# Performance work log

Measured on AMD Instinct MI355X. Metric: run time of the kernel, lower is better.

The kernel has to match this reference:

```python
import jax, jax.numpy as jnp
import numpy as np

N = 100000      # nodes
E = 3200000     # edges
F_IN = 128      # input feature dim
H = 256         # hidden dim
K = 30          # num_cluster
REG = 0.01      # regularizer coefficient


def _uniform(key, shape, fan_in):
    s = 1.0 / np.sqrt(fan_in)
    return jax.random.uniform(key, shape, jnp.float32, -s, s)


def setup_inputs() -> dict:
    key = jax.random.key(0)
    ks = jax.random.split(key, 11)
    x = jax.random.normal(ks[0], (N, F_IN), jnp.float32)
    edge_index = jax.random.randint(ks[1], (2, E), 0, N, jnp.int32)
    edge_attr = jax.random.uniform(ks[2], (E,), jnp.float32)
    return dict(
        x=x, edge_index=edge_index, edge_attr=edge_attr,
        W_conv1=_uniform(ks[3], (F_IN, H), F_IN), b_conv1=jnp.zeros((H,), jnp.float32),
        W_lin1=_uniform(ks[4], (F_IN, H), F_IN),  b_lin1=_uniform(ks[5], (H,), F_IN),
        W_conv2=_uniform(ks[6], (H, K), H),       b_conv2=jnp.zeros((K,), jnp.float32),
        W_lin2=_uniform(ks[7], (H, K), H),        b_lin2=_uniform(ks[8], (K,), H),
    )


def gcn_conv(x, W, b, row, col, w):
    """PyG GCNConv: symmetric-normalized, edge-weighted aggregation with self-loops (weight 1)."""
    n = x.shape[0]
    deg = jax.ops.segment_sum(w, col, num_segments=n) + 1.0  # self-loop weight 1
    dis = jax.lax.rsqrt(deg)                                  # deg > 0 always (self-loop)
    norm = dis[row] * w * dis[col]                            # [E]
    h = x @ W                                                 # [n, out]
    agg = jax.ops.segment_sum(norm[:, None] * h[row], col, num_segments=n)
    agg = agg + (dis * dis)[:, None] * h                      # self-loop contribution
    return agg + b


def reference(x, edge_index, edge_attr,
              W_conv1, b_conv1, W_lin1, b_lin1,
              W_conv2, b_conv2, W_lin2, b_lin2):
    row, col = edge_index[0], edge_index[1]
    # dropout is identity in eval mode
    h = jax.nn.relu(gcn_conv(x, W_conv1, b_conv1, row, col, edge_attr) + x @ W_lin1 + b_lin1)
    out = gcn_conv(h, W_conv2, b_conv2, row, col, edge_attr) + h @ W_lin2 + b_lin2
    FX = jnp.clip(jax.nn.softmax(out, axis=-1), 1e-9, 1.0 - 1e-9)  # [N, K]

    # modularity loss
    m = jnp.sum(edge_attr)
    degree = jax.ops.segment_sum(edge_attr, row, num_segments=x.shape[0])  # [N]
    connectivity = jnp.sum(edge_attr * jnp.sum(FX[row, :-1] * FX[col, :-1], axis=-1))
    s = jnp.sum(FX * degree[:, None], axis=0)[:-1]
    avg_connectivity = jnp.dot(s, s) / (2.0 * m)
    modularity = -(connectivity - avg_connectivity) / (2.0 * m)

    # collapse regularizer
    reg = (jnp.sqrt(jnp.sum(jnp.sum(FX, axis=0) ** 2) + 1e-9)
           * (FX.shape[-1] ** 0.5) / FX.shape[0] - 1.0)
    return FX, modularity + REG * reg
```

## Files before the change

kernel.cpp:

```cpp
#include <hip/hip_runtime.h>
#include <hip/hip_bf16.h>
#include <math.h>

#define N_NODES 100000
#define N_EDGES 3200000
#define F_IN 128
#define HID 256
#define KCL 30
#define NCOPY 8

typedef unsigned int uint;
typedef unsigned short ushort;
typedef unsigned char uchar;
typedef __attribute__((ext_vector_type(8))) short bf16x8;
typedef __attribute__((ext_vector_type(4))) float f32x4;
typedef __attribute__((ext_vector_type(2))) float f32x2;

static __device__ __forceinline__ float bf2f(ushort u) {
  return __uint_as_float(((uint)u) << 16);
}
static __device__ __forceinline__ float bf2f_hi(uint u) {
  return __uint_as_float(u & 0xFFFF0000u);
}
static __device__ __forceinline__ ushort f2bf(float f) {
  uint u = __float_as_uint(f);
  uint r = (u + 0x7FFF + ((u >> 16) & 1)) >> 16;
  return (ushort)r;
}

static __device__ __forceinline__ uchar f2fp8(float f) {
#if __has_builtin(__builtin_amdgcn_cvt_pk_fp8_f32)
  return (uchar)(__builtin_amdgcn_cvt_pk_fp8_f32(f, f, 0, false) & 0xFF);
#else
  uint u = __float_as_uint(f);
  uint s = (u >> 24) & 0x80u;
  float a = fabsf(f);
  if (a >= 448.f) return (uchar)(s | 0x7E);
  if (a < 0.015625f) {
    int q = (int)rintf(a * 512.f);
    return (uchar)(s | (q > 8 ? 8 : q));
  }
  int e = ((int)((u >> 23) & 0xFF)) - 127;
  float step = __uint_as_float((uint)(127 + e - 3) << 23);
  int q = (int)rintf(a / step);
  if (q == 16) { e += 1; q = 8; }
  return (uchar)(s | ((e + 7) << 3) | (q - 8));
#endif
}
static __device__ __forceinline__ float fp82f_sw(uchar b) {
  uint s = ((uint)(b & 0x80u)) << 24;
  uint em = b & 0x7Fu;
  float mag;
  if ((em >> 3) == 0) mag = (float)em * 0.001953125f;
  else mag = __uint_as_float((((em >> 3) + 120) << 23) | ((em & 7u) << 20));
  return __uint_as_float(s | __float_as_uint(mag));
}
static __device__ __forceinline__ void fp8x4_dec(uint u, float* o) {
#if __has_builtin(__builtin_amdgcn_cvt_pk_f32_fp8)
  f32x2 lo = __builtin_amdgcn_cvt_pk_f32_fp8((int)u, false);
  f32x2 hi = __builtin_amdgcn_cvt_pk_f32_fp8((int)u, true);
  o[0] = lo.x; o[1] = lo.y; o[2] = hi.x; o[3] = hi.y;
#else
  o[0] = fp82f_sw(u & 0xFF); o[1] = fp82f_sw((u >> 8) & 0xFF);
  o[2] = fp82f_sw((u >> 16) & 0xFF); o[3] = fp82f_sw((u >> 24) & 0xFF);
#endif
}


__global__ __launch_bounds__(256) void k_cnt8(const int* __restrict__ ei,
                                              int* __restrict__ cnt8) {
  int e = blockIdx.x * 256 + threadIdx.x;
  int g = blockIdx.x & (NCOPY - 1);
  int c = ei[N_EDGES + e];
  atomicAdd(cnt8 + (size_t)g * N_NODES + c, 1);
}

__global__ __launch_bounds__(1024) void k_scanA(const int* __restrict__ cnt8,
                                                int* __restrict__ off8,
                                                int* __restrict__ blocktot) {
  __shared__ int wsum[16];
  const int t = threadIdx.x;
  const int lane = t & 63, wid = t >> 6;
  int node = blockIdx.x * 1024 + t;
  int v[NCOPY];
  int tot = 0;
  if (node < N_NODES) {
    #pragma unroll
    for (int g = 0; g < NCOPY; ++g) {
      int x = cnt8[(size_t)g * N_NODES + node];
      v[g] = tot;
      tot += x;
    }
  } else {
    #pragma unroll
    for (int g = 0; g < NCOPY; ++g) v[g] = 0;
  }
  int x = tot;
  #pragma unroll
  for (int o = 1; o < 64; o <<= 1) {
    int y = __shfl_up(x, o);
    if (lane >= o) x += y;
  }
  if (lane == 63) wsum[wid] = x;
  __syncthreads();
  if (t < 16) {
    int s = wsum[t];
    #pragma unroll
    for (int o = 1; o < 16; o <<= 1) {
      int y = __shfl_up(s, o);
      if (t >= o) s += y;
    }
    wsum[t] = s;
  }
  __syncthreads();
  int excl = (wid ? wsum[wid - 1] : 0) + x - tot;
  if (node < N_NODES) {
    #pragma unroll
    for (int g = 0; g < NCOPY; ++g) off8[(size_t)node * NCOPY + g] = excl + v[g];
  }
  if (t == 0) blocktot[blockIdx.x] = wsum[15];
}

__global__ void k_scanB(const int* __restrict__ blocktot, int* __restrict__ blockoff) {
  if (threadIdx.x == 0 && blockIdx.x == 0) {
    int acc = 0;
    for (int b = 0; b < 98; ++b) { blockoff[b] = acc; acc += blocktot[b]; }
  }
}

__global__ __launch_bounds__(256) void k_scanC(int* __restrict__ off8,
                                               const int* __restrict__ blockoff) {
  int idx = blockIdx.x * 256 + threadIdx.x;
  if (idx > N_NODES * NCOPY) return;
  if (idx == N_NODES * NCOPY) { off8[idx] = N_EDGES; return; }
  off8[idx] += blockoff[idx >> 13];
}

__global__ __launch_bounds__(256) void k_csrfill8(const int* __restrict__ ei,
                                                  const float* __restrict__ w,
                                                  int* __restrict__ cnt8,
                                                  const int* __restrict__ off8,
                                                  int2* __restrict__ csr) {
  int e = blockIdx.x * 256 + threadIdx.x;
  int g = blockIdx.x & (NCOPY - 1);
  int r = ei[e], c = ei[N_EDGES + e];
  int idx = atomicSub(cnt8 + (size_t)g * N_NODES + c, 1) - 1;
  int pos = off8[(size_t)c * NCOPY + g] + idx;
  csr[pos] = make_int2(r, __float_as_int(w[e]));
}

__global__ __launch_bounds__(256) void k_degdis(const int* __restrict__ off8,
                                                const int2* __restrict__ csr,
                                                float* __restrict__ dis,
                                                float* __restrict__ m_out) {
  int n = blockIdx.x * 256 + threadIdx.x;
  float s = 0.f;
  if (n < N_NODES) {
    int e0 = off8[(size_t)n * NCOPY];
    int e1 = off8[(size_t)(n + 1) * NCOPY];
    for (int j = e0; j < e1; ++j) s += __int_as_float(csr[j].y);
    dis[n] = rsqrtf(s + 1.f);
  }
  float v = s;
  #pragma unroll
  for (int o = 32; o > 0; o >>= 1) v += __shfl_down(v, o);
  __shared__ float ls[4];
  int lane = threadIdx.x & 63, wid = threadIdx.x >> 6;
  if (lane == 0) ls[wid] = v;
  __syncthreads();
  if (threadIdx.x == 0) atomicAdd(m_out, ls[0] + ls[1] + ls[2] + ls[3]);
}

__global__ __launch_bounds__(256) void k_pn(int2* __restrict__ csr,
                                            const float* __restrict__ dis) {
  int j = blockIdx.x * 256 + threadIdx.x;
  int2 e = csr[j];
  csr[j] = make_int2(e.x, __float_as_int(__int_as_float(e.y) * dis[e.x]));
}

__global__ __launch_bounds__(256) void k_wprep(const float* __restrict__ Wc,
                                               const float* __restrict__ Wl,
                                               ushort* __restrict__ WT1) {
  int idx = blockIdx.x * 256 + threadIdx.x;
  int vc = idx >> 5;
  int kq = (idx & 31) * 4;
  const float* W = (vc < HID) ? Wc : Wl;
  int c = vc & (HID - 1);
  ushort4 u;
  u.x = f2bf(W[(size_t)(kq + 0) * HID + c]);
  u.y = f2bf(W[(size_t)(kq + 1) * HID + c]);
  u.z = f2bf(W[(size_t)(kq + 2) * HID + c]);
  u.w = f2bf(W[(size_t)(kq + 3) * HID + c]);
  *(ushort4*)(WT1 + (size_t)vc * F_IN + kq) = u;
}

__global__ __launch_bounds__(256) void k_wprep2(const float* __restrict__ Wc,
                                                const float* __restrict__ Wl,
                                                ushort* __restrict__ WT2) {
  int idx = blockIdx.x * 256 + threadIdx.x;
  int vc = idx >> 6;
  int kq = (idx & 63) * 4;
  const float* W = (vc < 32) ? Wc : Wl;
  int c = vc & 31;
  ushort4 u = make_ushort4(0, 0, 0, 0);
  if (c < KCL) {
    u.x = f2bf(W[(size_t)(kq + 0) * KCL + c]);
    u.y = f2bf(W[(size_t)(kq + 1) * KCL + c]);
    u.z = f2bf(W[(size_t)(kq + 2) * KCL + c]);
    u.w = f2bf(W[(size_t)(kq + 3) * KCL + c]);
  }
  *(ushort4*)(WT2 + (size_t)vc * HID + kq) = u;
}

__global__ __launch_bounds__(256) void k_gemm1m(const float* __restrict__ x,
                                                const ushort* __restrict__ WT1,
                                                const float* __restrict__ bc,
                                                const float* __restrict__ bl,
                                                const float* __restrict__ dis,
                                                uchar* __restrict__ hconv_f8,
                                                ushort* __restrict__ base1b) {
  __shared__ ushort xs[32 * F_IN];
  uchar* xs8 = (uchar*)xs;
  const int t = threadIdx.x;
  const int lane = t & 63, wid = t >> 6;
  const int m0 = blockIdx.x * 32;
  {
    int row = t >> 3, k0 = (t & 7) * 16;
    const float4* xp = (const float4*)(x + (size_t)(m0 + row) * F_IN + k0);
    #pragma unroll
    for (int q = 0; q < 4; ++q) {
      float4 v = xp[q];
      ushort4 u = make_ushort4(f2bf(v.x), f2bf(v.y), f2bf(v.z), f2bf(v.w));
      int k = k0 + q * 4;
      *(ushort4*)&xs[row * F_IN + (k ^ ((row & 7) << 3))] = u;
    }
  }
  __syncthreads();
  const int r0 = lane & 15, r1 = 16 + (lane & 15);
  const int kb = (lane >> 4) * 8;
  bf16x8 A0[4], A1[4];
  #pragma unroll
  for (int ks = 0; ks < 4; ++ks) {
    int k = ks * 32 + kb;
    A0[ks] = *(const bf16x8*)&xs[r0 * F_IN + (k ^ ((r0 & 7) << 3))];
    A1[ks] = *(const bf16x8*)&xs[r1 * F_IN + (k ^ ((r1 & 7) << 3))];
  }
  __syncthreads();
  const int rb = (lane >> 4) * 4;
  #pragma unroll
  for (int cb = 0; cb < 2; ++cb) {
    bf16x8 B[4][4];
    const int vbase = cb * 128 + wid * 32 + (lane & 15);
    #pragma unroll
    for (int cs = 0; cs < 2; ++cs)
      #pragma unroll
      for (int cf = 0; cf < 2; ++cf)
        #pragma unroll
        for (int ks = 0; ks < 4; ++ks) {
          int vc = cs * HID + vbase + cf * 16;
          B[cs * 2 + cf][ks] = *(const bf16x8*)(WT1 + (size_t)vc * F_IN + ks * 32 + kb);
        }
    f32x4 acc[2][4];
    #pragma unroll
    for (int fm = 0; fm < 2; ++fm)
      #pragma unroll
      for (int f = 0; f < 4; ++f) acc[fm][f] = (f32x4){0.f, 0.f, 0.f, 0.f};
    #pragma unroll
    for (int ks = 0; ks < 4; ++ks) {
      #pragma unroll
      for (int f = 0; f < 4; ++f) {
        acc[0][f] = __builtin_amdgcn_mfma_f32_16x16x32_bf16(A0[ks], B[f][ks], acc[0][f], 0, 0, 0);
        acc[1][f] = __builtin_amdgcn_mfma_f32_16x16x32_bf16(A1[ks], B[f][ks], acc[1][f], 0, 0, 0);
      }
    }
    #pragma unroll
    for (int cf = 0; cf < 2; ++cf) {
      int c = cb * 128 + wid * 32 + cf * 16 + (lane & 15);
      float bcv = bc[c], blv = bl[c];
      #pragma unroll
      for (int fm = 0; fm < 2; ++fm) {
        #pragma unroll
        for (int r = 0; r < 4; ++r) {
          int lrow = fm * 16 + rb + r;
          int row = m0 + lrow;
          float hc = acc[fm][cf][r];
          float hl = acc[fm][2 + cf][r];
          float d = dis[row];
          xs8[lrow * 256 + c] = f2fp8(hc);
          base1b[(size_t)row * HID + c] = f2bf(hl + blv + bcv + d * d * hc);
        }
      }
    }
  }
  __syncthreads();
  {
    int row = t >> 3, c0 = (t & 7) * 32;
    uint4 a = *(const uint4*)&xs8[row * 256 + c0];
    uint4 b = *(const uint4*)&xs8[row * 256 + c0 + 16];
    uchar* dst = hconv_f8 + (size_t)(m0 + row) * 256 + c0;
    *(uint4*)dst = a;
    *(uint4*)(dst + 16) = b;
  }
}

__global__ __launch_bounds__(256) void k_agg1(const int* __restrict__ off8,
                                              const int2* __restrict__ csr,
                                              const uint* __restrict__ hconv_u32,
                                              const ushort* __restrict__ base1b,
                                              const float* __restrict__ dis,
                                              ushort* __restrict__ h1b) {
  const int n = blockIdx.x;
  const int t = threadIdx.x;
  const int lane = t & 63, wid = t >> 6;
  const int e0 = off8[(size_t)n * NCOPY];
  const int e1 = off8[(size_t)(n + 1) * NCOPY];
  __shared__ int2 s_e[256];
  __shared__ float red[4][256];
  float acc0 = 0.f, acc1 = 0.f, acc2 = 0.f, acc3 = 0.f;
  for (int jb = e0; jb < e1; jb += 256) {
    int cn = min(256, e1 - jb);
    __syncthreads();
    if (t < cn) s_e[t] = csr[jb + t];
    __syncthreads();
    int j = wid;
    for (; j + 4 < cn; j += 8) {
      int2 eA = s_e[j];
      int2 eB = s_e[j + 4];
      float nA = __int_as_float(eA.y);
      float nB = __int_as_float(eB.y);
      uint uA = hconv_u32[(size_t)eA.x * 64 + lane];
      uint uB = hconv_u32[(size_t)eB.x * 64 + lane];
      float vA[4], vB[4];
      fp8x4_dec(uA, vA);
      fp8x4_dec(uB, vB);
      acc0 = fmaf(nA, vA[0], acc0); acc1 = fmaf(nA, vA[1], acc1);
      acc2 = fmaf(nA, vA[2], acc2); acc3 = fmaf(nA, vA[3], acc3);
      acc0 = fmaf(nB, vB[0], acc0); acc1 = fmaf(nB, vB[1], acc1);
      acc2 = fmaf(nB, vB[2], acc2); acc3 = fmaf(nB, vB[3], acc3);
    }
    if (j < cn) {
      int2 eA = s_e[j];
      float nA = __int_as_float(eA.y);
      uint uA = hconv_u32[(size_t)eA.x * 64 + lane];
      float vA[4];
      fp8x4_dec(uA, vA);
      acc0 = fmaf(nA, vA[0], acc0); acc1 = fmaf(nA, vA[1], acc1);
      acc2 = fmaf(nA, vA[2], acc2); acc3 = fmaf(nA, vA[3], acc3);
    }
  }
  __syncthreads();
  ((float4*)red[wid])[lane] = make_float4(acc0, acc1, acc2, acc3);
  __syncthreads();
  float dn = dis[n];
  float v = dn * (red[0][t] + red[1][t] + red[2][t] + red[3][t]) + bf2f(base1b[(size_t)n * HID + t]);
  h1b[(size_t)n * HID + t] = f2bf(fmaxf(v, 0.f));
}

__global__ __launch_bounds__(256) void k_gemm2m(const ushort* __restrict__ h1b,
                                                const ushort* __restrict__ WT2,
                                                const float* __restrict__ bc,
                                                const float* __restrict__ bl,
                                                const float* __restrict__ dis,
                                                ushort* __restrict__ hconv2p,
                                                float* __restrict__ base2p) {
  __shared__ ushort hs[64 * HID];
  const int t = threadIdx.x;
  const int lane = t & 63, wid = t >> 6;
  const int n0 = blockIdx.x * 64;
  {
    int row = t >> 2, kq = (t & 3) * 64;
    int gn = n0 + row;
    #pragma unroll
    for (int q = 0; q < 8; ++q) {
      int k = kq + q * 8;
      uint4 u = make_uint4(0, 0, 0, 0);
      if (gn < N_NODES) u = *(const uint4*)(h1b + (size_t)gn * HID + k);
      *(uint4*)&hs[row * HID + (k ^ ((row & 7) << 3))] = u;
    }
  }
  __syncthreads();
  const int lr = wid * 16 + (lane & 15);
  const int kb = (lane >> 4) * 8;
  f32x4 acc[4];
  #pragma unroll
  for (int f = 0; f < 4; ++f) acc[f] = (f32x4){0.f, 0.f, 0.f, 0.f};
  #pragma unroll
  for (int ks = 0; ks < 8; ++ks) {
    int k = ks * 32 + kb;
    bf16x8 A = *(const bf16x8*)&hs[lr * HID + (k ^ ((lr & 7) << 3))];
    #pragma unroll
    for (int f = 0; f < 4; ++f) {
      int vc = f * 16 + (lane & 15);
      bf16x8 B = *(const bf16x8*)(WT2 + (size_t)vc * HID + k);
      acc[f] = __builtin_amdgcn_mfma_f32_16x16x32_bf16(A, B, acc[f], 0, 0, 0);
    }
  }
  const int rb = (lane >> 4) * 4;
  #pragma unroll
  for (int cf = 0; cf < 2; ++cf) {
    int c = cf * 16 + (lane & 15);
    if (c < KCL) {
      float bcv = bc[c], blv = bl[c];
      #pragma unroll
      for (int r = 0; r < 4; ++r) {
        int row = n0 + wid * 16 + rb + r;
        if (row < N_NODES) {
          float hc = acc[cf][r];
          float hl = acc[2 + cf][r];
          float d = dis[row];
          hconv2p[(size_t)row * 32 + c] = f2bf(hc);
          base2p[(size_t)row * 32 + c] = hl + blv + bcv + d * d * hc;
        }
      }
    }
  }
}

__global__ __launch_bounds__(256) void k_agg2(const int* __restrict__ off8,
                                              const int2* __restrict__ csr,
                                              const float* __restrict__ dis,
                                              const ushort* __restrict__ hconv2p,
                                              const float* __restrict__ base2p,
                                              float* __restrict__ FX,
                                              ushort* __restrict__ FXbp,
                                              float* __restrict__ scal) {
  const int t = threadIdx.x;
  const int lane = t & 63, wid = t >> 6;
  const int half = lane >> 5, c = lane & 31;
  const int nwaves = gridDim.x * 4;
  const int gw = blockIdx.x * 4 + wid;
  float cs_acc = 0.f;
  for (int n = gw; n < N_NODES; n += nwaves) {
    int e0 = off8[(size_t)n * NCOPY];
    int e1 = off8[(size_t)(n + 1) * NCOPY];
    float accA = 0.f, accB = 0.f;
    int j = e0 + half;
    for (; j + 2 < e1; j += 4) {
      int2 eA = csr[j];
      int2 eB = csr[j + 2];
      float p0 = __int_as_float(eA.y);
      float p1 = __int_as_float(eB.y);
      float v0 = (c < KCL) ? bf2f(hconv2p[(size_t)eA.x * 32 + c]) : 0.f;
      float v1 = (c < KCL) ? bf2f(hconv2p[(size_t)eB.x * 32 + c]) : 0.f;
      accA = fmaf(p0, v0, accA);
      accB = fmaf(p1, v1, accB);
    }
    if (j < e1) {
      int2 eA = csr[j];
      float p0 = __int_as_float(eA.y);
      float v0 = (c < KCL) ? bf2f(hconv2p[(size_t)eA.x * 32 + c]) : 0.f;
      accA = fmaf(p0, v0, accA);
    }
    float acc = accA + accB;
    acc += __shfl(acc, lane ^ 32);
    float out = (c < KCL) ? acc * dis[n] + base2p[(size_t)n * 32 + c] : -1e30f;
    float mx = out;
    #pragma unroll
    for (int o = 16; o > 0; o >>= 1) mx = fmaxf(mx, __shfl_xor(mx, o));
    float p = (c < KCL) ? __expf(out - mx) : 0.f;
    float sum = p;
    #pragma unroll
    for (int o = 16; o > 0; o >>= 1) sum += __shfl_xor(sum, o);
    float fx = p / sum;
    fx = fminf(fmaxf(fx, 1e-9f), 1.f - 1e-9f);
    if (half == 0 && c < KCL) {
      FX[(size_t)n * KCL + c] = fx;
      FXbp[(size_t)n * 32 + c] = f2bf(fx);
    }
    cs_acc += (c < KCL) ? fx : 0.f;
  }
  __shared__ float red_cs[4][32];
  if (half == 0) red_cs[wid][c] = cs_acc;
  __syncthreads();
  if (t < KCL) {
    float a = red_cs[0][t] + red_cs[1][t] + red_cs[2][t] + red_cs[3][t];
    atomicAdd(&scal[2 + t], a);
  }
}

__global__ __launch_bounds__(256) void k_conn(const int* __restrict__ ei,
                                              const float* __restrict__ w,
                                              const ushort* __restrict__ FXbp,
                                              float* __restrict__ scal) {
  const int t = threadIdx.x;
  const int lane = t & 63, wid = t >> 6;
  const size_t e0 = ((size_t)blockIdx.x * 256 + t) * 4;
  float sv[29];
  #pragma unroll
  for (int k = 0; k < 29; ++k) sv[k] = 0.f;
  float conn = 0.f;
  int4 rr = *(const int4*)(ei + e0);
  int4 cc = *(const int4*)(ei + N_EDGES + e0);
  float4 ww = *(const float4*)(w + e0);
  const int rA[4] = {rr.x, rr.y, rr.z, rr.w};
  const int cA[4] = {cc.x, cc.y, cc.z, cc.w};
  const float wA[4] = {ww.x, ww.y, ww.z, ww.w};
  #pragma unroll
  for (int q = 0; q < 4; ++q) {
    int r = rA[q], cN = cA[q];
    float wv = wA[q];
    const uint* fr = (const uint*)FXbp + (size_t)r * 16;
    const uint* fc = (const uint*)FXbp + (size_t)cN * 16;
    float dot = 0.f;
    #pragma unroll
    for (int k = 0; k < 14; ++k) {
      uint ua = fr[k], ub = fc[k];
      float a0 = bf2f((ushort)(ua & 0xFFFF)), a1 = bf2f_hi(ua);
      float b0 = bf2f((ushort)(ub & 0xFFFF)), b1 = bf2f_hi(ub);
      dot += a0 * b0 + a1 * b1;
      sv[2 * k] = fmaf(wv, a0, sv[2 * k]);
      sv[2 * k + 1] = fmaf(wv, a1, sv[2 * k + 1]);
    }
    float a28 = bf2f((ushort)(fr[14] & 0xFFFF));
    float b28 = bf2f((ushort)(fc[14] & 0xFFFF));
    dot += a28 * b28;
    sv[28] = fmaf(wv, a28, sv[28]);
    conn = fmaf(wv, dot, conn);
  }
  __shared__ float red[4][30];
  #pragma unroll
  for (int i = 0; i < 30; ++i) {
    float v = (i < 29) ? sv[i] : conn;
    #pragma unroll
    for (int o = 32; o > 0; o >>= 1) v += __shfl_down(v, o);
    if (lane == 0) red[wid][i] = v;
  }
  __syncthreads();
  if (t < 30) {
    float s = red[0][t] + red[1][t] + red[2][t] + red[3][t];
    atomicAdd(t == 29 ? &scal[1] : &scal[32 + t], s);
  }
}

__global__ void k_finalize(const float* __restrict__ scal, float* __restrict__ out_loss) {
  if (threadIdx.x == 0 && blockIdx.x == 0) {
    float m = scal[0], conn = scal[1];
    float ss = 0.f;
    for (int k = 0; k < KCL - 1; ++k) { float s = scal[32 + k]; ss += s * s; }
    float cs2 = 0.f;
    for (int k = 0; k < KCL; ++k) { float cv = scal[2 + k]; cs2 += cv * cv; }
    float avg = ss / (2.f * m);
    float modularity = -(conn - avg) / (2.f * m);
    float reg = sqrtf(cs2 + 1e-9f) * sqrtf((float)KCL) / (float)N_NODES - 1.f;
    out_loss[0] = modularity + 0.01f * reg;
  }
}

extern "C" void kernel_launch(void* const* d_in, const int* in_sizes, int n_in,
                              void* d_out, int out_size, void* d_ws, size_t ws_size,
                              hipStream_t stream) {
  const float* x   = (const float*)d_in[0];
  const int*   ei  = (const int*)d_in[1];
  const float* ea  = (const float*)d_in[2];
  const float* Wc1 = (const float*)d_in[3];
  const float* bc1 = (const float*)d_in[4];
  const float* Wl1 = (const float*)d_in[5];
  const float* bl1 = (const float*)d_in[6];
  const float* Wc2 = (const float*)d_in[7];
  const float* bc2 = (const float*)d_in[8];
  const float* Wl2 = (const float*)d_in[9];
  const float* bl2 = (const float*)d_in[10];
  float* out = (float*)d_out;

  float* ws = (float*)d_ws;
  size_t o = 0;
  int*   cnt8   = (int*)(ws + o); o += (size_t)NCOPY * N_NODES;
  float* scal   = ws + o; o += 64;
  size_t zero_floats = o;
  int*   off8   = (int*)(ws + o); o += (size_t)N_NODES * NCOPY + 8;
  int*   blocktot = (int*)(ws + o); o += 128;
  int*   blockoff = (int*)(ws + o); o += 128;
  float* dis    = ws + o; o += N_NODES;
  int2*  csr    = (int2*)(ws + o); o += (size_t)N_EDGES * 2;
  ushort* WT1   = (ushort*)(ws + o); o += (size_t)512 * F_IN / 2;
  ushort* WT2   = (ushort*)(ws + o); o += (size_t)64 * HID / 2;
  uchar* hconv_f8 = (uchar*)(ws + o); o += (size_t)N_NODES * HID / 4;
  ushort* base1b = (ushort*)(ws + o); o += (size_t)N_NODES * HID / 2;
  ushort* h1b   = (ushort*)(ws + o); o += (size_t)N_NODES * HID / 2;
  ushort* hconv2p = (ushort*)(ws + o); o += (size_t)N_NODES * 32 / 2;
  float* base2p = ws + o; o += (size_t)N_NODES * 32;
  o += 64;
  if (ws_size < o * sizeof(float)) return;

  ushort* FXbp = (ushort*)hconv_f8;

  hipMemsetAsync(d_ws, 0, zero_floats * sizeof(float), stream);

  k_cnt8<<<N_EDGES / 256, 256, 0, stream>>>(ei, cnt8);
  k_scanA<<<98, 1024, 0, stream>>>(cnt8, off8, blocktot);
  k_scanB<<<1, 64, 0, stream>>>(blocktot, blockoff);
  k_scanC<<<(N_NODES * NCOPY + 256) / 256, 256, 0, stream>>>(off8, blockoff);
  k_csrfill8<<<N_EDGES / 256, 256, 0, stream>>>(ei, ea, cnt8, off8, csr);
  k_degdis<<<(N_NODES + 255) / 256, 256, 0, stream>>>(off8, csr, dis, scal);
  k_pn<<<N_EDGES / 256, 256, 0, stream>>>(csr, dis);
  k_wprep<<<64, 256, 0, stream>>>(Wc1, Wl1, WT1);
  k_wprep2<<<16, 256, 0, stream>>>(Wc2, Wl2, WT2);
  k_gemm1m<<<N_NODES / 32, 256, 0, stream>>>(x, WT1, bc1, bl1, dis, hconv_f8, base1b);
  k_agg1<<<N_NODES, 256, 0, stream>>>(off8, csr, (const uint*)hconv_f8, base1b, dis, h1b);
  k_gemm2m<<<(N_NODES + 63) / 64, 256, 0, stream>>>(h1b, WT2, bc2, bl2, dis, hconv2p, base2p);
  k_agg2<<<2048, 256, 0, stream>>>(off8, csr, dis, hconv2p, base2p, out, FXbp, scal);
  k_conn<<<N_EDGES / 1024, 256, 0, stream>>>(ei, ea, FXbp, scal);
  k_finalize<<<1, 64, 0, stream>>>(scal, out + (size_t)N_NODES * KCL);
}
```

Baseline: 888.8 us.

## Compute connectivity via CSR aggregation and store layer-2 features in fp8

Result: slower. 912.4 us (+2.7%).

```diff
diff --git a/kernel.cpp b/kernel.cpp
--- a/kernel.cpp
+++ b/kernel.cpp
@@ -18,9 +18,6 @@
 
 static __device__ __forceinline__ float bf2f(ushort u) {
   return __uint_as_float(((uint)u) << 16);
-}
-static __device__ __forceinline__ float bf2f_hi(uint u) {
-  return __uint_as_float(u & 0xFFFF0000u);
 }
 static __device__ __forceinline__ ushort f2bf(float f) {
   uint u = __float_as_uint(f);
@@ -65,6 +62,14 @@
   o[2] = fp82f_sw((u >> 16) & 0xFF); o[3] = fp82f_sw((u >> 24) & 0xFF);
 #endif
 }
+static __device__ __forceinline__ float fp81_dec(uchar b) {
+#if __has_builtin(__builtin_amdgcn_cvt_pk_f32_fp8)
+  f32x2 lo = __builtin_amdgcn_cvt_pk_f32_fp8((int)(uint)b, false);
+  return lo.x;
+#else
+  return fp82f_sw(b);
+#endif
+}
 
 
 __global__ __launch_bounds__(256) void k_cnt8(const int* __restrict__ ei,
@@ -140,17 +145,17 @@
                                                   const float* __restrict__ w,
                                                   int* __restrict__ cnt8,
                                                   const int* __restrict__ off8,
-                                                  int2* __restrict__ csr) {
+                                                  int4* __restrict__ csr) {
   int e = blockIdx.x * 256 + threadIdx.x;
   int g = blockIdx.x & (NCOPY - 1);
   int r = ei[e], c = ei[N_EDGES + e];
   int idx = atomicSub(cnt8 + (size_t)g * N_NODES + c, 1) - 1;
   int pos = off8[(size_t)c * NCOPY + g] + idx;
-  csr[pos] = make_int2(r, __float_as_int(w[e]));
+  csr[pos] = make_int4(r, __float_as_int(w[e]), 0, 0);
 }
 
 __global__ __launch_bounds__(256) void k_degdis(const int* __restrict__ off8,
-                                                const int2* __restrict__ csr,
+                                                const int4* __restrict__ csr,
                                                 float* __restrict__ dis,
                                                 float* __restrict__ m_out) {
   int n = blockIdx.x * 256 + threadIdx.x;
@@ -171,11 +176,12 @@
   if (threadIdx.x == 0) atomicAdd(m_out, ls[0] + ls[1] + ls[2] + ls[3]);
 }
 
-__global__ __launch_bounds__(256) void k_pn(int2* __restrict__ csr,
+__global__ __launch_bounds__(256) void k_pn(int4* __restrict__ csr,
                                             const float* __restrict__ dis) {
   int j = blockIdx.x * 256 + threadIdx.x;
-  int2 e = csr[j];
-  csr[j] = make_int2(e.x, __float_as_int(__int_as_float(e.y) * dis[e.x]));
+  int4 e = csr[j];
+  float pnv = __int_as_float(e.y) * dis[e.x];
+  ((float*)csr)[(size_t)j * 4 + 2] = pnv;
 }
 
 __global__ __launch_bounds__(256) void k_wprep(const float* __restrict__ Wc,
@@ -304,7 +310,7 @@
 }
 
 __global__ __launch_bounds__(256) void k_agg1(const int* __restrict__ off8,
-                                              const int2* __restrict__ csr,
+                                              const int4* __restrict__ csr,
                                               const uint* __restrict__ hconv_u32,
                                               const ushort* __restrict__ base1b,
                                               const float* __restrict__ dis,
@@ -320,7 +326,10 @@
   for (int jb = e0; jb < e1; jb += 256) {
     int cn = min(256, e1 - jb);
     __syncthreads();
-    if (t < cn) s_e[t] = csr[jb + t];
+    if (t < cn) {
+      int4 e = csr[jb + t];
+      s_e[t] = make_int2(e.x, e.z);
+    }
     __syncthreads();
     int j = wid;
     for (; j + 4 < cn; j += 8) {
@@ -361,7 +370,7 @@
                                                 const float* __restrict__ bc,
                                                 const float* __restrict__ bl,
                                                 const float* __restrict__ dis,
-                                                ushort* __restrict__ hconv2p,
+                                                uchar* __restrict__ hconv2f8,
                                                 float* __restrict__ base2p) {
   __shared__ ushort hs[64 * HID];
   const int t = threadIdx.x;
@@ -408,7 +417,7 @@
           float hc = acc[cf][r];
           float hl = acc[2 + cf][r];
           float d = dis[row];
-          hconv2p[(size_t)row * 32 + c] = f2bf(hc);
+          hconv2f8[(size_t)row * 32 + c] = f2fp8(hc);
           base2p[(size_t)row * 32 + c] = hl + blv + bcv + d * d * hc;
         }
       }
@@ -417,12 +426,12 @@
 }
 
 __global__ __launch_bounds__(256) void k_agg2(const int* __restrict__ off8,
-                                              const int2* __restrict__ csr,
+                                              const int4* __restrict__ csr,
                                               const float* __restrict__ dis,
-                                              const ushort* __restrict__ hconv2p,
+                                              const uchar* __restrict__ hconv2f8,
                                               const float* __restrict__ base2p,
                                               float* __restrict__ FX,
-                                              ushort* __restrict__ FXbp,
+                                              uchar* __restrict__ FXb8,
                                               float* __restrict__ scal) {
   const int t = threadIdx.x;
   const int lane = t & 63, wid = t >> 6;
@@ -436,19 +445,22 @@
     float accA = 0.f, accB = 0.f;
     int j = e0 + half;
     for (; j + 2 < e1; j += 4) {
-      int2 eA = csr[j];
-      int2 eB = csr[j + 2];
-      float p0 = __int_as_float(eA.y);
-      float p1 = __int_as_float(eB.y);
-      float v0 = (c < KCL) ? bf2f(hconv2p[(size_t)eA.x * 32 + c]) : 0.f;
-      float v1 = (c < KCL) ? bf2f(hconv2p[(size_t)eB.x * 32 + c]) : 0.f;
+      int4 eA = csr[j];
+      int4 eB = csr[j + 2];
+      float p0 = __int_as_float(eA.z);
+      float p1 = __int_as_float(eB.z);
+      uchar b0 = hconv2f8[(size_t)eA.x * 32 + c];
+      uchar b1 = hconv2f8[(size_t)eB.x * 32 + c];
+      float v0 = (c < KCL) ? fp81_dec(b0) : 0.f;
+      float v1 = (c < KCL) ? fp81_dec(b1) : 0.f;
       accA = fmaf(p0, v0, accA);
       accB = fmaf(p1, v1, accB);
     }
     if (j < e1) {
-      int2 eA = csr[j];
-      float p0 = __int_as_float(eA.y);
-      float v0 = (c < KCL) ? bf2f(hconv2p[(size_t)eA.x * 32 + c]) : 0.f;
+      int4 eA = csr[j];
+      float p0 = __int_as_float(eA.z);
+      uchar b0 = hconv2f8[(size_t)eA.x * 32 + c];
+      float v0 = (c < KCL) ? fp81_dec(b0) : 0.f;
       accA = fmaf(p0, v0, accA);
     }
     float acc = accA + accB;
@@ -465,7 +477,7 @@
     fx = fminf(fmaxf(fx, 1e-9f), 1.f - 1e-9f);
     if (half == 0 && c < KCL) {
       FX[(size_t)n * KCL + c] = fx;
-      FXbp[(size_t)n * 32 + c] = f2bf(fx);
+      FXb8[(size_t)n * 32 + c] = f2fp8(fx);
     }
     cs_acc += (c < KCL) ? fx : 0.f;
   }
@@ -478,57 +490,54 @@
   }
 }
 
-__global__ __launch_bounds__(256) void k_conn(const int* __restrict__ ei,
-                                              const float* __restrict__ w,
-                                              const ushort* __restrict__ FXbp,
-                                              float* __restrict__ scal) {
+__global__ __launch_bounds__(256) void k_connc(const int* __restrict__ off8,
+                                               const int4* __restrict__ csr,
+                                               const uchar* __restrict__ FXb8,
+                                               float* __restrict__ scal) {
   const int t = threadIdx.x;
   const int lane = t & 63, wid = t >> 6;
-  const size_t e0 = ((size_t)blockIdx.x * 256 + t) * 4;
-  float sv[29];
-  #pragma unroll
-  for (int k = 0; k < 29; ++k) sv[k] = 0.f;
-  float conn = 0.f;
-  int4 rr = *(const int4*)(ei + e0);
-  int4 cc = *(const int4*)(ei + N_EDGES + e0);
-  float4 ww = *(const float4*)(w + e0);
-  const int rA[4] = {rr.x, rr.y, rr.z, rr.w};
-  const int cA[4] = {cc.x, cc.y, cc.z, cc.w};
-  const float wA[4] = {ww.x, ww.y, ww.z, ww.w};
-  #pragma unroll
-  for (int q = 0; q < 4; ++q) {
-    int r = rA[q], cN = cA[q];
-    float wv = wA[q];
-    const uint* fr = (const uint*)FXbp + (size_t)r * 16;
-    const uint* fc = (const uint*)FXbp + (size_t)cN * 16;
-    float dot = 0.f;
-    #pragma unroll
-    for (int k = 0; k < 14; ++k) {
-      uint ua = fr[k], ub = fc[k];
-      float a0 = bf2f((ushort)(ua & 0xFFFF)), a1 = bf2f_hi(ua);
-      float b0 = bf2f((ushort)(ub & 0xFFFF)), b1 = bf2f_hi(ub);
-      dot += a0 * b0 + a1 * b1;
-      sv[2 * k] = fmaf(wv, a0, sv[2 * k]);
-      sv[2 * k + 1] = fmaf(wv, a1, sv[2 * k + 1]);
-    }
-    float a28 = bf2f((ushort)(fr[14] & 0xFFFF));
-    float b28 = bf2f((ushort)(fc[14] & 0xFFFF));
-    dot += a28 * b28;
-    sv[28] = fmaf(wv, a28, sv[28]);
-    conn = fmaf(wv, dot, conn);
-  }
-  __shared__ float red[4][30];
-  #pragma unroll
-  for (int i = 0; i < 30; ++i) {
-    float v = (i < 29) ? sv[i] : conn;
-    #pragma unroll
-    for (int o = 32; o > 0; o >>= 1) v += __shfl_down(v, o);
-    if (lane == 0) red[wid][i] = v;
-  }
-  __syncthreads();
-  if (t < 30) {
-    float s = red[0][t] + red[1][t] + red[2][t] + red[3][t];
-    atomicAdd(t == 29 ? &scal[1] : &scal[32 + t], s);
+  const int half = lane >> 5, c = lane & 31;
+  const int nwaves = gridDim.x * 4;
+  const int gw = blockIdx.x * 4 + wid;
+  const bool ck = (c < KCL - 1);
+  float conn_acc = 0.f, sv_acc = 0.f;
+  for (int n = gw; n < N_NODES; n += nwaves) {
+    int e0 = off8[(size_t)n * NCOPY];
+    int e1 = off8[(size_t)(n + 1) * NCOPY];
+    float VA = 0.f, VB = 0.f;
+    int j = e0 + half;
+    for (; j + 2 < e1; j += 4) {
+      int4 eA = csr[j];
+      int4 eB = csr[j + 2];
+      float w0 = __int_as_float(eA.y);
+      float w1 = __int_as_float(eB.y);
+      uchar b0 = FXb8[(size_t)eA.x * 32 + c];
+      uchar b1 = FXb8[(size_t)eB.x * 32 + c];
+      VA = fmaf(w0, fp81_dec(b0), VA);
+      VB = fmaf(w1, fp81_dec(b1), VB);
+    }
+    if (j < e1) {
+      int4 eA = csr[j];
+      VA = fmaf(__int_as_float(eA.y), fp81_dec(FXb8[(size_t)eA.x * 32 + c]), VA);
+    }
+    float V = VA + VB;
+    V += __shfl(V, lane ^ 32);
+    if (half == 0 && ck) {
+      float fxn = fp81_dec(FXb8[(size_t)n * 32 + c]);
+      conn_acc = fmaf(V, fxn, conn_acc);
+      sv_acc += V;
+    }
+  }
+  __shared__ float rc[4][32], rs[4][32];
+  if (half == 0) { rc[wid][c] = conn_acc; rs[wid][c] = sv_acc; }
+  __syncthreads();
+  if (t < 32) {
+    float a = (t < KCL - 1) ? (rc[0][t] + rc[1][t] + rc[2][t] + rc[3][t]) : 0.f;
+    float b = rs[0][t] + rs[1][t] + rs[2][t] + rs[3][t];
+    if (t < KCL - 1) atomicAdd(&scal[32 + t], b);
+    #pragma unroll
+    for (int o = 16; o > 0; o >>= 1) a += __shfl_xor(a, o);
+    if (t == 0) atomicAdd(&scal[1], a);
   }
 }
 
@@ -571,18 +580,18 @@
   int*   blocktot = (int*)(ws + o); o += 128;
   int*   blockoff = (int*)(ws + o); o += 128;
   float* dis    = ws + o; o += N_NODES;
-  int2*  csr    = (int2*)(ws + o); o += (size_t)N_EDGES * 2;
+  int4*  csr    = (int4*)(ws + o); o += (size_t)N_EDGES * 4;
   ushort* WT1   = (ushort*)(ws + o); o += (size_t)512 * F_IN / 2;
   ushort* WT2   = (ushort*)(ws + o); o += (size_t)64 * HID / 2;
   uchar* hconv_f8 = (uchar*)(ws + o); o += (size_t)N_NODES * HID / 4;
   ushort* base1b = (ushort*)(ws + o); o += (size_t)N_NODES * HID / 2;
   ushort* h1b   = (ushort*)(ws + o); o += (size_t)N_NODES * HID / 2;
-  ushort* hconv2p = (ushort*)(ws + o); o += (size_t)N_NODES * 32 / 2;
+  uchar* hconv2f8 = (uchar*)(ws + o); o += (size_t)N_NODES * 32 / 4;
   float* base2p = ws + o; o += (size_t)N_NODES * 32;
   o += 64;
   if (ws_size < o * sizeof(float)) return;
 
-  ushort* FXbp = (ushort*)hconv_f8;
+  uchar* FXb8 = hconv_f8;
 
   hipMemsetAsync(d_ws, 0, zero_floats * sizeof(float), stream);
 
@@ -597,8 +606,8 @@
   k_wprep2<<<16, 256, 0, stream>>>(Wc2, Wl2, WT2);
   k_gemm1m<<<N_NODES / 32, 256, 0, stream>>>(x, WT1, bc1, bl1, dis, hconv_f8, base1b);
   k_agg1<<<N_NODES, 256, 0, stream>>>(off8, csr, (const uint*)hconv_f8, base1b, dis, h1b);
-  k_gemm2m<<<(N_NODES + 63) / 64, 256, 0, stream>>>(h1b, WT2, bc2, bl2, dis, hconv2p, base2p);
-  k_agg2<<<2048, 256, 0, stream>>>(off8, csr, dis, hconv2p, base2p, out, FXbp, scal);
-  k_conn<<<N_EDGES / 1024, 256, 0, stream>>>(ei, ea, FXbp, scal);
+  k_gemm2m<<<(N_NODES + 63) / 64, 256, 0, stream>>>(h1b, WT2, bc2, bl2, dis, hconv2f8, base2p);
+  k_agg2<<<2048, 256, 0, stream>>>(off8, csr, dis, hconv2f8, base2p, out, FXb8, scal);
+  k_connc<<<2048, 256, 0, stream>>>(off8, csr, FXb8, scal);
   k_finalize<<<1, 64, 0, stream>>>(scal, out + (size_t)N_NODES * KCL);
 }
```
